# Optimization experiments

Measured on AMD Instinct MI355X. Metric: run time of the kernel, lower is better.

The kernel has to match this reference:

```python
import jax, jax.numpy as jnp
import numpy as np

N, D, H, E = 8192, 1024, 4096, 8


def setup_inputs() -> dict:
    key = jax.random.key(0)
    ks = jax.random.split(key, 5)
    s_in = 1.0 / np.sqrt(D)
    s_h = 1.0 / np.sqrt(H)
    return {
        "x": jax.random.normal(ks[0], (N, D), dtype=jnp.float32),
        "Wg": jax.random.normal(ks[1], (D, E), dtype=jnp.float32) * s_in,
        "bg": jnp.zeros((E,), dtype=jnp.float32),
        "W1": jax.random.normal(ks[2], (E, D, H), dtype=jnp.float32) * s_in,
        "b1": jnp.zeros((E, H), dtype=jnp.float32),
        "W2": jax.random.normal(ks[3], (E, H, D), dtype=jnp.float32) * s_h,
        "b2": jnp.zeros((E, D), dtype=jnp.float32),
    }


def reference(x, Wg, bg, W1, b1, W2, b2):
    # gate: softmax linear router -> weights [N, E]
    weights = jax.nn.softmax(x @ Wg + bg, axis=-1)
    # all experts, batched GEMMs: h [N, E, H]
    h = jax.nn.relu(jnp.einsum("nd,edh->neh", x, W1) + b1)  # Dropout is identity at inference
    outputs = jnp.einsum("neh,ehd->ned", h, W2) + b2         # [N, E, D]
    # weighted combine over experts
    return jnp.einsum("ne,ned->nd", weights, outputs)
```

## Files before the change

### kernel.cpp

```cpp
#include <hip/hip_runtime.h>
#include <hip/hip_bf16.h>

#define DDIM 1024
#define HDIM 4096
#define NEXP 8
#define NROW 8192
#define KPAIR 8192

typedef __attribute__((ext_vector_type(8))) short s16x8;
typedef __attribute__((ext_vector_type(4))) float f32x4;

using bf16 = __hip_bfloat16;

__device__ __forceinline__ void gload16(const bf16* g, bf16* lds) {
    __builtin_amdgcn_global_load_lds(
        (const __attribute__((address_space(1))) unsigned int*)g,
        (__attribute__((address_space(3))) unsigned int*)lds,
        16, 0, 0);
}

template <int N>
__device__ __forceinline__ void wait_vmcnt() {
    if constexpr (N == 6)      asm volatile("s_waitcnt vmcnt(6)" ::: "memory");
    else if constexpr (N == 3) asm volatile("s_waitcnt vmcnt(3)" ::: "memory");
    else                       asm volatile("s_waitcnt vmcnt(0)" ::: "memory");
}

__global__ void cvtgate_kernel(const float* __restrict__ x, const float* __restrict__ Wg,
                               const float* __restrict__ bg, const float* __restrict__ b2,
                               bf16* __restrict__ xb, float* __restrict__ wts,
                               float* __restrict__ out) {
    int wave = threadIdx.x >> 6, lane = threadIdx.x & 63;
    int n = blockIdx.x * 4 + wave;
    const float* xr = x + (size_t)n * DDIM;
    bf16* xbr = xb + (size_t)n * DDIM;
    float acc[NEXP] = {0.f, 0.f, 0.f, 0.f, 0.f, 0.f, 0.f, 0.f};
#pragma unroll
    for (int j = 0; j < 4; ++j) {
        int d0 = j * 256 + lane * 4;
        float4 v = *(const float4*)&xr[d0];
        union { bf16 b[4]; uint2 u; } pk;
        pk.b[0] = __float2bfloat16(v.x);
        pk.b[1] = __float2bfloat16(v.y);
        pk.b[2] = __float2bfloat16(v.z);
        pk.b[3] = __float2bfloat16(v.w);
        *(uint2*)&xbr[d0] = pk.u;
        const float* w0 = Wg + (size_t)d0 * NEXP;
#pragma unroll
        for (int e = 0; e < NEXP; ++e)
            acc[e] += v.x * w0[e] + v.y * w0[NEXP + e] + v.z * w0[2 * NEXP + e] +
                      v.w * w0[3 * NEXP + e];
    }
#pragma unroll
    for (int off = 32; off > 0; off >>= 1) {
#pragma unroll
        for (int e = 0; e < NEXP; ++e) acc[e] += __shfl_xor(acc[e], off, 64);
    }
    float mx = -1e30f;
#pragma unroll
    for (int e = 0; e < NEXP; ++e) { acc[e] += bg[e]; mx = fmaxf(mx, acc[e]); }
    float s = 0.f;
#pragma unroll
    for (int e = 0; e < NEXP; ++e) { acc[e] = __expf(acc[e] - mx); s += acc[e]; }
    float inv = 1.0f / s;
#pragma unroll
    for (int e = 0; e < NEXP; ++e) acc[e] *= inv;
    if (lane == 0) {
#pragma unroll
        for (int e = 0; e < NEXP; ++e) wts[(size_t)n * NEXP + e] = acc[e];
    }
    float* outr = out + (size_t)n * DDIM;
#pragma unroll
    for (int j = 0; j < 4; ++j) {
        int d0 = j * 256 + lane * 4;
        float4 sum = {0.f, 0.f, 0.f, 0.f};
#pragma unroll
        for (int e = 0; e < NEXP; ++e) {
            float4 bv = *(const float4*)&b2[(size_t)e * DDIM + d0];
            sum.x += acc[e] * bv.x;
            sum.y += acc[e] * bv.y;
            sum.z += acc[e] * bv.z;
            sum.w += acc[e] * bv.w;
        }
        *(float4*)&outr[d0] = sum;
    }
}

__global__ void transpose_pair_kernel(const float* __restrict__ W1s, bf16* __restrict__ W1d,
                                      const float* __restrict__ W2s, bf16* __restrict__ W2d) {
    __shared__ float t[128][65];
    const int z = blockIdx.z;
    const float* src; bf16* dst; int C, ldo, bx, by;
    if (z < 2) {
        src = W1s + (size_t)z * DDIM * HDIM;
        dst = W1d + (size_t)z * HDIM * DDIM;
        C = HDIM; ldo = DDIM;
        bx = blockIdx.x & 31; by = blockIdx.x >> 5;
    } else {
        src = W2s + (size_t)(z - 2) * HDIM * DDIM;
        dst = W2d + (size_t)(z - 2) * HDIM;
        C = DDIM; ldo = KPAIR;
        bx = blockIdx.x & 7; by = blockIdx.x >> 3;
    }
    const int r0 = by * 64, c0 = bx * 128;
    const int tid = threadIdx.x;
    const int lrow = tid >> 5, lc4 = tid & 31;
#pragma unroll
    for (int i = 0; i < 8; ++i) {
        int rr = i * 8 + lrow;
        float4 v = *(const float4*)&src[(size_t)(r0 + rr) * C + c0 + lc4 * 4];
        t[lc4 * 4 + 0][rr] = v.x;
        t[lc4 * 4 + 1][rr] = v.y;
        t[lc4 * 4 + 2][rr] = v.z;
        t[lc4 * 4 + 3][rr] = v.w;
    }
    __syncthreads();
    const int oc = tid >> 3, oj = tid & 7;
#pragma unroll
    for (int i = 0; i < 4; ++i) {
        int c = oc + i * 32;
        union { bf16 b[8]; s16x8 v; } p;
#pragma unroll
        for (int q = 0; q < 8; ++q) p.b[q] = __float2bfloat16(t[c][oj * 8 + q]);
        *(s16x8*)&dst[(size_t)(c0 + c) * ldo + r0 + oj * 8] = p.v;
    }
}

__global__ __launch_bounds__(512, 1) void gemm1(
    const bf16* __restrict__ A, const bf16* __restrict__ BTp, bf16* __restrict__ Hsb,
    const float* __restrict__ b1p, const float* __restrict__ wts,
    int lda, int ldb, int ldc, int NT, int tilesM, int tilesN, int XGN, int e0) {
    constexpr int WROWS = 128;
    constexpr int HALFA = 256 * 32;
    constexpr int HALFB = 256 * 32;
    constexpr int ATOT = 2 * HALFA;
    constexpr int BUFE = ATOT + 2 * HALFB;
    __shared__ __align__(16) bf16 smem[2 * BUFE];

    const int tid = threadIdx.x;
    const int wave = tid >> 6, lane = tid & 63;
    const int wm = wave >> 2, wn = wave & 3;
    const int r = lane & 15, kg = lane >> 4;

    const int eh = blockIdx.x >> 9;
    const int bx = blockIdx.x & 511;
    const bf16* BT = BTp + (size_t)eh * HDIM * DDIM;
    bf16* Cout = Hsb + (size_t)eh * HDIM;
    const float* bias = b1p + (size_t)eh * HDIM;
    const int expert = e0 + eh;

    const int xcd = bx & 7, slot = bx >> 3;
    const int XGM = 8 / XGN;
    const int rm = tilesM / XGM, rn = tilesN / XGN;
    const int g = slot >> 5, u = slot & 31;
    const int gpr = rn >> 3;
    const int gm = (g / gpr) * 4 + (u >> 3);
    const int gn = (g % gpr) * 8 + (u & 7);
    const int tm = (xcd / XGN) * rm + gm;
    const int tn = (xcd % XGN) * rn + gn;

    const bf16* gA = A + (size_t)tm * 256 * lda;
    const bf16* gB = BT + (size_t)tn * 256 * ldb;

    f32x4 acc[8][4];
#pragma unroll
    for (int m = 0; m < 8; ++m)
#pragma unroll
        for (int n = 0; n < 4; ++n) acc[m][n] = (f32x4){0.f, 0.f, 0.f, 0.f};

    auto stageA = [&](int t, int ks) {
        bf16* dst = smem + (t & 1) * BUFE + ks * HALFA;
#pragma unroll
        for (int j = 0; j < 2; ++j) {
            int c = j * 512 + tid;
            int R = c >> 2, kc = (c & 3) ^ ((R >> 1) & 3);
            gload16(gA + (size_t)R * lda + t * 64 + ks * 32 + kc * 8,
                    dst + (j * 512 + wave * 64) * 8);
        }
    };
    auto stageB = [&](int t, int ks) {
        bf16* dst = smem + (t & 1) * BUFE + ATOT + ks * HALFB;
#pragma unroll
        for (int j = 0; j < 2; ++j) {
            int c = j * 512 + tid;
            int R = c >> 2, kc = (c & 3) ^ ((R >> 1) & 3);
            gload16(gB + (size_t)R * ldb + t * 64 + ks * 32 + kc * 8,
                    dst + (j * 512 + wave * 64) * 8);
        }
    };

    s16x8 a0[4], bb[4];
    auto ldA = [&](int buf, int ks, int mh) {
#pragma unroll
        for (int m = 0; m < 4; ++m) {
            int R = wm * WROWS + mh * 64 + m * 16 + r;
            a0[m] = *(const s16x8*)&smem[buf * BUFE + ks * HALFA + R * 32 +
                                         ((kg ^ ((R >> 1) & 3)) * 8)];
        }
    };
    auto ldB = [&](int buf, int ks) {
#pragma unroll
        for (int n = 0; n < 4; ++n) {
            int R = wn * 64 + n * 16 + r;
            bb[n] = *(const s16x8*)&smem[buf * BUFE + ATOT + ks * HALFB + R * 32 +
                                         ((kg ^ ((R >> 1) & 3)) * 8)];
        }
    };

    auto preMFMA = [&]() {
        __builtin_amdgcn_s_barrier();
        asm volatile("s_waitcnt lgkmcnt(0)" ::: "memory");
        __builtin_amdgcn_sched_barrier(0);
        __builtin_amdgcn_s_setprio(1);
    };
    auto postMFMA = [&](bool vm) {
        __builtin_amdgcn_s_setprio(0);
        if (vm) wait_vmcnt<6>();
        __builtin_amdgcn_s_barrier();
    };
    auto mfmaLo = [&]() {
#pragma unroll
        for (int m = 0; m < 4; ++m)
#pragma unroll
            for (int n = 0; n < 4; ++n)
                acc[m][n] = __builtin_amdgcn_mfma_f32_16x16x32_bf16(a0[m], bb[n], acc[m][n], 0, 0, 0);
    };
    auto mfmaHi = [&]() {
#pragma unroll
        for (int m = 0; m < 4; ++m)
#pragma unroll
            for (int n = 0; n < 4; ++n)
                acc[4 + m][n] = __builtin_amdgcn_mfma_f32_16x16x32_bf16(a0[m], bb[n], acc[4 + m][n], 0, 0, 0);
    };

    stageB(0, 0); stageA(0, 0); stageB(0, 1); stageA(0, 1);
    stageB(1, 0); stageA(1, 0); stageB(1, 1);
    wait_vmcnt<6>();
    __builtin_amdgcn_s_barrier();

    const int NI = NT / 2;
    for (int i = 0; i < NI; ++i) {
        const int t0 = 2 * i, t1 = t0 + 1;
        const bool g2 = (t0 + 2 < NT), g3 = (t1 + 2 < NT);
        ldB(0, 0); ldA(0, 0, 0); stageA(t1, 1);
        preMFMA(); mfmaLo(); postMFMA(false);
        ldA(0, 0, 1); if (g2) stageB(t0 + 2, 0);
        preMFMA(); mfmaHi(); postMFMA(false);
        ldB(0, 1); ldA(0, 1, 0); if (g2) stageA(t0 + 2, 0);
        preMFMA(); mfmaLo(); postMFMA(false);
        ldA(0, 1, 1); if (g2) stageB(t0 + 2, 1);
        preMFMA(); mfmaHi(); postMFMA(true);
        ldB(1, 0); ldA(1, 0, 0); if (g2) stageA(t0 + 2, 1);
        preMFMA(); mfmaLo(); postMFMA(false);
        ldA(1, 0, 1); if (g3) stageB(t1 + 2, 0);
        preMFMA(); mfmaHi(); postMFMA(false);
        ldB(1, 1); ldA(1, 1, 0); if (g3) stageA(t1 + 2, 0);
        preMFMA(); mfmaLo(); postMFMA(false);
        ldA(1, 1, 1); if (g3) stageB(t1 + 2, 1);
        preMFMA(); mfmaHi(); postMFMA(true);
    }

    bf16* hs = smem;
    const int col0 = tn * 256 + wn * 64;
#pragma unroll
    for (int n = 0; n < 4; ++n) {
        float bv = bias[col0 + n * 16 + r];
        int cl = wn * 64 + n * 16 + r;
#pragma unroll
        for (int mf = 0; mf < 8; ++mf) {
#pragma unroll
            for (int j = 0; j < 4; ++j) {
                int rl = wm * WROWS + (mf >> 2) * 64 + (mf & 3) * 16 + kg * 4 + j;
                float wv = wts[((size_t)tm * 256 + rl) * NEXP + expert];
                float v = acc[mf][n][j] + bv;
                v = v > 0.f ? v : 0.f;
                hs[rl * 256 + (cl ^ ((rl & 7) << 3))] = __float2bfloat16(wv * v);
            }
        }
    }
    __builtin_amdgcn_s_barrier();
    asm volatile("s_waitcnt lgkmcnt(0)" ::: "memory");
    const size_t rbase = (size_t)tm * 256;
    const int cbase = tn * 256;
#pragma unroll
    for (int i2 = 0; i2 < 16; ++i2) {
        int rl = wave * 32 + i2 * 2 + (lane >> 5);
        int c8 = (lane & 31) * 8;
        s16x8 v = *(const s16x8*)&hs[rl * 256 + (c8 ^ ((rl & 7) << 3))];
        *(s16x8*)&Cout[(rbase + rl) * (size_t)ldc + cbase + c8] = v;
    }
}

__global__ __launch_bounds__(256, 2) void gemm2p(
    const bf16* __restrict__ A, const bf16* __restrict__ BT, float* __restrict__ O,
    int lda, int ldb, int ldc, int NT, int tilesM, int tilesN, int XGN) {
    constexpr int HALFA = 128 * 32;
    constexpr int HALFB = 128 * 32;
    constexpr int ATOT = 2 * HALFA;
    constexpr int BUFE = ATOT + 2 * HALFB;
    constexpr int RSTR = 68;
    __shared__ __align__(16) bf16 smem[2 * BUFE];

    const int tid = threadIdx.x;
    const int wave = tid >> 6, lane = tid & 63;
    const int ksw = wave & 1, wn = wave >> 1;
    const int r = lane & 15, kg = lane >> 4;

    const int xcd = blockIdx.x & 7, slot = blockIdx.x >> 3;
    const int XGM = 8 / XGN;
    const int rm = tilesM / XGM, rn = tilesN / XGN;
    const int g = slot >> 5, u = slot & 31;
    const int gpr = rn >> 3;
    const int gm = (g / gpr) * 4 + (u >> 3);
    const int gn = (g % gpr) * 8 + (u & 7);
    const int tm = (xcd / XGN) * rm + gm;
    const int tn = (xcd % XGN) * rn + gn;

    const bf16* gA = A + (size_t)tm * 128 * lda;
    const bf16* gB = BT + (size_t)tn * 128 * ldb;

    f32x4 acc[8][4];
#pragma unroll
    for (int m = 0; m < 8; ++m)
#pragma unroll
        for (int n = 0; n < 4; ++n) acc[m][n] = (f32x4){0.f, 0.f, 0.f, 0.f};

    auto stageA_rh = [&](int t, int rh) {
        bf16* base = smem + (t & 1) * BUFE;
#pragma unroll
        for (int j = 0; j < 2; ++j) {
            int c = j * 256 + tid;
            int Rl = (c >> 2) & 63;
            int R = rh * 64 + Rl;
            int kc = (c & 3) ^ ((R >> 1) & 3);
            gload16(gA + (size_t)R * lda + t * 64 + j * 32 + kc * 8,
                    base + j * HALFA + rh * 2048 + ((c & 255) - lane) * 8 + lane * 8);
        }
    };
    auto stageB = [&](int t) {
        bf16* base = smem + (t & 1) * BUFE + ATOT;
#pragma unroll
        for (int j = 0; j < 4; ++j) {
            int c = j * 256 + tid;
            int ks = c >> 9;
            int R = (c >> 2) & 127;
            int kc = (c & 3) ^ ((R >> 1) & 3);
            gload16(gB + (size_t)R * ldb + t * 64 + ks * 32 + kc * 8,
                    base + ks * HALFB + ((c & 511) - lane) * 8 + lane * 8);
        }
    };

    s16x8 a0[4], a1[4], bfr[4];
    auto ldA0 = [&](int b) {
#pragma unroll
        for (int m = 0; m < 4; ++m) {
            int R = m * 16 + r;
            a0[m] = *(const s16x8*)&smem[b * BUFE + ksw * HALFA + R * 32 +
                                         ((kg ^ ((R >> 1) & 3)) * 8)];
        }
    };
    auto ldA1 = [&](int b) {
#pragma unroll
        for (int m = 0; m < 4; ++m) {
            int R = 64 + m * 16 + r;
            a1[m] = *(const s16x8*)&smem[b * BUFE + ksw * HALFA + R * 32 +
                                         ((kg ^ ((R >> 1) & 3)) * 8)];
        }
    };
    auto ldB = [&](int b) {
#pragma unroll
        for (int n = 0; n < 4; ++n) {
            int R = wn * 64 + n * 16 + r;
            bfr[n] = *(const s16x8*)&smem[b * BUFE + ATOT + ksw * HALFB + R * 32 +
                                          ((kg ^ ((R >> 1) & 3)) * 8)];
        }
    };

    stageA_rh(0, 0); stageA_rh(0, 1); stageB(0);
    wait_vmcnt<0>();
    __builtin_amdgcn_s_barrier();

    for (int t = 0; t < NT; ++t) {
        const int b = t & 1;
        ldB(b); ldA1(b); ldA0(b);
        if (t + 1 < NT) { stageA_rh(t + 1, 0); stageA_rh(t + 1, 1); stageB(t + 1); }
        asm volatile("s_waitcnt lgkmcnt(4)" ::: "memory");
        __builtin_amdgcn_sched_barrier(0);
        __builtin_amdgcn_s_setprio(1);
#pragma unroll
        for (int m = 0; m < 4; ++m)
#pragma unroll
            for (int n = 0; n < 4; ++n)
                acc[4 + m][n] = __builtin_amdgcn_mfma_f32_16x16x32_bf16(a1[m], bfr[n], acc[4 + m][n], 0, 0, 0);
        __builtin_amdgcn_s_setprio(0);
        asm volatile("s_waitcnt lgkmcnt(0)" ::: "memory");
        __builtin_amdgcn_sched_barrier(0);
        __builtin_amdgcn_s_setprio(1);
#pragma unroll
        for (int m = 0; m < 4; ++m)
#pragma unroll
            for (int n = 0; n < 4; ++n)
                acc[m][n] = __builtin_amdgcn_mfma_f32_16x16x32_bf16(a0[m], bfr[n], acc[m][n], 0, 0, 0);
        __builtin_amdgcn_s_setprio(0);
        if (t + 1 < NT) {
            wait_vmcnt<0>();
            __builtin_amdgcn_s_barrier();
        }
    }

    __syncthreads();
    float* red = (float*)smem;
    const int zone = wn * (64 * RSTR);
    const int col0 = tn * 128 + wn * 64;
    const size_t row0 = (size_t)tm * 128;
    if (ksw == 1) {
#pragma unroll
        for (int mq = 0; mq < 4; ++mq)
#pragma unroll
            for (int n = 0; n < 4; ++n) {
                int rl = mq * 16 + kg * 4;
                int cl = n * 16 + r;
#pragma unroll
                for (int j = 0; j < 4; ++j)
                    red[zone + (rl + j) * RSTR + cl] = acc[mq][n][j];
            }
    }
    __syncthreads();
    if (ksw == 0) {
#pragma unroll
        for (int mq = 0; mq < 4; ++mq)
#pragma unroll
            for (int j = 0; j < 4; ++j) {
                int rl = mq * 16 + kg * 4 + j;
                size_t rr = row0 + rl;
#pragma unroll
                for (int n = 0; n < 4; ++n) {
                    int cl = n * 16 + r;
                    O[rr * (size_t)ldc + col0 + cl] += acc[mq][n][j] + red[zone + rl * RSTR + cl];
                }
            }
    }
    __syncthreads();
    if (ksw == 0) {
#pragma unroll
        for (int mq = 0; mq < 4; ++mq)
#pragma unroll
            for (int n = 0; n < 4; ++n) {
                int rl = mq * 16 + kg * 4;
                int cl = n * 16 + r;
#pragma unroll
                for (int j = 0; j < 4; ++j)
                    red[zone + (rl + j) * RSTR + cl] = acc[4 + mq][n][j];
            }
    }
    __syncthreads();
    if (ksw == 1) {
#pragma unroll
        for (int mq = 0; mq < 4; ++mq)
#pragma unroll
            for (int j = 0; j < 4; ++j) {
                int rl = mq * 16 + kg * 4 + j;
                size_t rr = row0 + 64 + rl;
#pragma unroll
                for (int n = 0; n < 4; ++n) {
                    int cl = n * 16 + r;
                    O[rr * (size_t)ldc + col0 + cl] += acc[4 + mq][n][j] + red[zone + rl * RSTR + cl];
                }
            }
    }
}

extern "C" void kernel_launch(void* const* d_in, const int* in_sizes, int n_in,
                              void* d_out, int out_size, void* d_ws, size_t ws_size,
                              hipStream_t stream) {
    const float* x  = (const float*)d_in[0];
    const float* Wg = (const float*)d_in[1];
    const float* bg = (const float*)d_in[2];
    const float* W1 = (const float*)d_in[3];
    const float* b1 = (const float*)d_in[4];
    const float* W2 = (const float*)d_in[5];
    const float* b2 = (const float*)d_in[6];
    float* out = (float*)d_out;

    char* ws = (char*)d_ws;
    bf16* xb   = (bf16*)(ws);
    bf16* W1P  = (bf16*)(ws + (16ull << 20));
    bf16* W2P  = (bf16*)(ws + (32ull << 20));
    bf16* Hs   = (bf16*)(ws + (48ull << 20));
    float* wts = (float*)(ws + (176ull << 20));

    cvtgate_kernel<<<NROW / 4, 256, 0, stream>>>(x, Wg, bg, b2, xb, wts, out);

    for (int p = 0; p < 4; ++p) {
        transpose_pair_kernel<<<dim3(512, 1, 4), 256, 0, stream>>>(
            W1 + (size_t)2 * p * DDIM * HDIM, W1P,
            W2 + (size_t)2 * p * HDIM * DDIM, W2P);
        gemm1<<<1024, 512, 0, stream>>>(
            xb, W1P, Hs, b1 + (size_t)2 * p * HDIM, wts,
            DDIM, DDIM, KPAIR, DDIM / 64, 32, 16, 2, 2 * p);
        gemm2p<<<512, 256, 0, stream>>>(
            Hs, W2P, out, KPAIR, KPAIR, DDIM, KPAIR / 64, 64, 8, 1);
    }
}
```

Baseline: 1.221 ms.

## Replace fine-grained barrier-pinned GEMM pipeline with per-tile double buffer loop

Replaces the hand-interleaved schedule, which issued global-to-LDS stages between eight barrier-fenced MFMA phases per two tiles, with a simpler loop. Each iteration prefetches the whole next tile, loads both A halves and B into separate registers, and uses partial lgkmcnt waits to overlap LDS reads with MFMAs. This removes most per-phase barriers but adds a full vmcnt(0) wait each tile and raises register use for the extra A fragment. That can expose global load latency and reduce occupancy.

```diff
diff --git a/kernel.cpp b/kernel.cpp
--- a/kernel.cpp
+++ b/kernel.cpp
@@ -189,13 +189,21 @@
         }
     };
 
-    s16x8 a0[4], bb[4];
-    auto ldA = [&](int buf, int ks, int mh) {
+    s16x8 aLo[4], aHi[4], bb[4];
+    auto ldALo = [&](int buf, int ks) {
 #pragma unroll
         for (int m = 0; m < 4; ++m) {
-            int R = wm * WROWS + mh * 64 + m * 16 + r;
-            a0[m] = *(const s16x8*)&smem[buf * BUFE + ks * HALFA + R * 32 +
-                                         ((kg ^ ((R >> 1) & 3)) * 8)];
+            int R = wm * WROWS + m * 16 + r;
+            aLo[m] = *(const s16x8*)&smem[buf * BUFE + ks * HALFA + R * 32 +
+                                          ((kg ^ ((R >> 1) & 3)) * 8)];
+        }
+    };
+    auto ldAHi = [&](int buf, int ks) {
+#pragma unroll
+        for (int m = 0; m < 4; ++m) {
+            int R = wm * WROWS + 64 + m * 16 + r;
+            aHi[m] = *(const s16x8*)&smem[buf * BUFE + ks * HALFA + R * 32 +
+                                          ((kg ^ ((R >> 1) & 3)) * 8)];
         }
     };
     auto ldB = [&](int buf, int ks) {
@@ -207,59 +215,57 @@
         }
     };
 
-    auto preMFMA = [&]() {
-        __builtin_amdgcn_s_barrier();
+    auto mfmaLo = [&]() {
+#pragma unroll
+        for (int m = 0; m < 4; ++m)
+#pragma unroll
+            for (int n = 0; n < 4; ++n)
+                acc[m][n] = __builtin_amdgcn_mfma_f32_16x16x32_bf16(aLo[m], bb[n], acc[m][n], 0, 0, 0);
+    };
+    auto mfmaHi = [&]() {
+#pragma unroll
+        for (int m = 0; m < 4; ++m)
+#pragma unroll
+            for (int n = 0; n < 4; ++n)
+                acc[4 + m][n] = __builtin_amdgcn_mfma_f32_16x16x32_bf16(aHi[m], bb[n], acc[4 + m][n], 0, 0, 0);
+    };
+
+    stageA(0, 0); stageB(0, 0); stageA(0, 1); stageB(0, 1);
+    wait_vmcnt<0>();
+    __builtin_amdgcn_s_barrier();
+
+    for (int t = 0; t < NT; ++t) {
+        const int b = t & 1;
+        if (t + 1 < NT) { stageA(t + 1, 0); stageB(t + 1, 0); stageA(t + 1, 1); stageB(t + 1, 1); }
+        ldB(b, 0); ldALo(b, 0); ldAHi(b, 0);
+        asm volatile("s_waitcnt lgkmcnt(4)" ::: "memory");
+        __builtin_amdgcn_sched_barrier(0);
+        __builtin_amdgcn_s_setprio(1);
+        mfmaLo();
+        __builtin_amdgcn_s_setprio(0);
         asm volatile("s_waitcnt lgkmcnt(0)" ::: "memory");
         __builtin_amdgcn_sched_barrier(0);
         __builtin_amdgcn_s_setprio(1);
-    };
-    auto postMFMA = [&](bool vm) {
+        mfmaHi();
         __builtin_amdgcn_s_setprio(0);
-        if (vm) wait_vmcnt<6>();
-        __builtin_amdgcn_s_barrier();
-    };
-    auto mfmaLo = [&]() {
-#pragma unroll
-        for (int m = 0; m < 4; ++m)
-#pragma unroll
-            for (int n = 0; n < 4; ++n)
-                acc[m][n] = __builtin_amdgcn_mfma_f32_16x16x32_bf16(a0[m], bb[n], acc[m][n], 0, 0, 0);
-    };
-    auto mfmaHi = [&]() {
-#pragma unroll
-        for (int m = 0; m < 4; ++m)
-#pragma unroll
-            for (int n = 0; n < 4; ++n)
-                acc[4 + m][n] = __builtin_amdgcn_mfma_f32_16x16x32_bf16(a0[m], bb[n], acc[4 + m][n], 0, 0, 0);
-    };
-
-    stageB(0, 0); stageA(0, 0); stageB(0, 1); stageA(0, 1);
-    stageB(1, 0); stageA(1, 0); stageB(1, 1);
-    wait_vmcnt<6>();
+        ldB(b, 1); ldALo(b, 1); ldAHi(b, 1);
+        asm volatile("s_waitcnt lgkmcnt(4)" ::: "memory");
+        __builtin_amdgcn_sched_barrier(0);
+        __builtin_amdgcn_s_setprio(1);
+        mfmaLo();
+        __builtin_amdgcn_s_setprio(0);
+        asm volatile("s_waitcnt lgkmcnt(0)" ::: "memory");
+        __builtin_amdgcn_sched_barrier(0);
+        __builtin_amdgcn_s_setprio(1);
+        mfmaHi();
+        __builtin_amdgcn_s_setprio(0);
+        if (t + 1 < NT) {
+            wait_vmcnt<0>();
+            __builtin_amdgcn_s_barrier();
+        }
+    }
+
     __builtin_amdgcn_s_barrier();
-
-    const int NI = NT / 2;
-    for (int i = 0; i < NI; ++i) {
-        const int t0 = 2 * i, t1 = t0 + 1;
-        const bool g2 = (t0 + 2 < NT), g3 = (t1 + 2 < NT);
-        ldB(0, 0); ldA(0, 0, 0); stageA(t1, 1);
-        preMFMA(); mfmaLo(); postMFMA(false);
-        ldA(0, 0, 1); if (g2) stageB(t0 + 2, 0);
-        preMFMA(); mfmaHi(); postMFMA(false);
-        ldB(0, 1); ldA(0, 1, 0); if (g2) stageA(t0 + 2, 0);
-        preMFMA(); mfmaLo(); postMFMA(false);
-        ldA(0, 1, 1); if (g2) stageB(t0 + 2, 1);
-        preMFMA(); mfmaHi(); postMFMA(true);
-        ldB(1, 0); ldA(1, 0, 0); if (g2) stageA(t0 + 2, 1);
-        preMFMA(); mfmaLo(); postMFMA(false);
-        ldA(1, 0, 1); if (g3) stageB(t1 + 2, 0);
-        preMFMA(); mfmaHi(); postMFMA(false);
-        ldB(1, 1); ldA(1, 1, 0); if (g3) stageA(t1 + 2, 0);
-        preMFMA(); mfmaLo(); postMFMA(false);
-        ldA(1, 1, 1); if (g3) stageB(t1 + 2, 1);
-        preMFMA(); mfmaHi(); postMFMA(true);
-    }
-
     bf16* hs = smem;
     const int col0 = tn * 256 + wn * 64;
 #pragma unroll
```

Result: no change. 1.225 ms, median of 2 (+0.3%).
